# Kernel optimization log

Measured on AMD Instinct MI355X. Metric: run time of the kernel, lower is better.

## Reference

```python
import jax, jax.numpy as jnp
import numpy as np

B, T, D = 64, 1024, 1024  # batch, seq_len, in_dim == out_dim
N_UNIT = 2


def _lstm_cell(x, h, c, Wih, Whh):
    # x:[B,Din], h,c:[B,D]; Wih:[4D,Din], Whh:[4D,D]  (PyTorch gate order i,f,g,o)
    gates = x @ Wih.T + h @ Whh.T           # [B,4D]
    i, f, g, o = jnp.split(gates, 4, axis=-1)
    i = jax.nn.sigmoid(i)
    f = jax.nn.sigmoid(f)
    g = jnp.tanh(g)
    o = jax.nn.sigmoid(o)
    c_new = f * c + i * g
    h_new = o * jnp.tanh(c_new)
    return h_new, c_new


def setup_inputs() -> dict:
    key = jax.random.key(0)
    ks = jax.random.split(key, 5)
    s_in = 1.0 / np.sqrt(D)
    x = jax.random.normal(ks[0], (B, T, D), dtype=jnp.float32)
    Wih0 = jax.random.normal(ks[1], (4 * D, D), dtype=jnp.float32) * s_in
    Whh0 = jax.random.normal(ks[2], (4 * D, D), dtype=jnp.float32) * s_in
    Wih1 = jax.random.normal(ks[3], (4 * D, D), dtype=jnp.float32) * s_in
    Whh1 = jax.random.normal(ks[4], (4 * D, D), dtype=jnp.float32) * s_in
    return {"x": x, "Wih0": Wih0, "Whh0": Whh0, "Wih1": Wih1, "Whh1": Whh1}


def reference(x, Wih0, Whh0, Wih1, Whh1):
    b = x.shape[0]
    d = Whh0.shape[1]
    z = jnp.zeros((b, d), dtype=x.dtype)
    # Original code seeds both h and c of every unit with the same zeros tensor.
    carry0 = (z, z, z, z)  # (h0, c0, h1, c1)

    def step(carry, xt):
        h0, c0, h1, c1 = carry
        h0, c0 = _lstm_cell(xt, h0, c0, Wih0, Whh0)
        h1, c1 = _lstm_cell(h0, h1, c1, Wih1, Whh1)
        return (h0, c0, h1, c1), h1

    xs = jnp.swapaxes(x, 0, 1)  # [T,B,D]
    _, outs = jax.lax.scan(step, carry0, xs)
    return jnp.swapaxes(outs, 0, 1)  # [B,T,D]
```

## Files before the change

kernel.cpp:

```cpp
#include <hip/hip_runtime.h>
#include <cstdint>
#include <cstddef>

#define B_ 64
#define T_ 1024
#define D_ 1024
#define NBLK 256

typedef __attribute__((ext_vector_type(8))) _Float16 half8;
typedef __attribute__((ext_vector_type(4))) float f32x4;
typedef unsigned int u32;
typedef unsigned long long u64;
typedef unsigned short u16;

static __device__ __forceinline__ f32x4 mfma16(half8 a, half8 b, f32x4 c) {
  return __builtin_amdgcn_mfma_f32_16x16x32_f16(a, b, c, 0, 0, 0);
}
static __device__ __forceinline__ u64 cohl64(const u64* p) {
  return __hip_atomic_load(p, __ATOMIC_RELAXED, __HIP_MEMORY_SCOPE_AGENT);
}
static __device__ __forceinline__ u32 cohl32(const u32* p) {
  return __hip_atomic_load(p, __ATOMIC_RELAXED, __HIP_MEMORY_SCOPE_AGENT);
}
static __device__ __forceinline__ void cohs32(u32* p, u32 v) {
  __hip_atomic_store(p, v, __ATOMIC_RELAXED, __HIP_MEMORY_SCOPE_AGENT);
}
static __device__ __forceinline__ u16 h2u(_Float16 h) {
  return __builtin_bit_cast(u16, h);
}


static __device__ __forceinline__ void stage_coh(const _Float16* src, u64* st, int tid) {
  const int r = tid >> 5, j = tid & 31;
  const u64* p0 = (const u64*)(src + (size_t)r * D_) + j * 2;
  const u64* p1 = (const u64*)(src + (size_t)(r + 16) * D_) + j * 2;
  #pragma unroll
  for (int k = 0; k < 4; ++k) {
    st[2 * k] = cohl64(p0 + k * 64);
    st[2 * k + 1] = cohl64(p0 + k * 64 + 1);
    st[8 + 2 * k] = cohl64(p1 + k * 64);
    st[8 + 2 * k + 1] = cohl64(p1 + k * 64 + 1);
  }
}
static __device__ __forceinline__ void stage_x(const _Float16* src, u64* st, int tid) {
  const int r = tid >> 5, j = tid & 31;
  const u64* p0 = (const u64*)(src + (size_t)r * T_ * D_) + j * 2;
  const u64* p1 = (const u64*)(src + (size_t)(r + 16) * T_ * D_) + j * 2;
  #pragma unroll
  for (int k = 0; k < 4; ++k) {
    st[2 * k] = p0[k * 64];
    st[2 * k + 1] = p0[k * 64 + 1];
    st[8 + 2 * k] = p1[k * 64];
    st[8 + 2 * k + 1] = p1[k * 64 + 1];
  }
}
static __device__ __forceinline__ void stage_xf(const float* src, u64* st, int tid) {
  const int r = tid >> 5, j = tid & 31;
  #pragma unroll
  for (int h = 0; h < 2; ++h) {
    const float4* p = (const float4*)(src + (size_t)(r + h * 16) * T_ * D_) + j * 2;
    #pragma unroll
    for (int k = 0; k < 4; ++k) {
      #pragma unroll
      for (int q = 0; q < 2; ++q) {
        float4 v = p[k * 64 + q];
        union { u16 us[4]; u64 u; } pk;
        pk.us[0] = h2u((_Float16)v.x); pk.us[1] = h2u((_Float16)v.y);
        pk.us[2] = h2u((_Float16)v.z); pk.us[3] = h2u((_Float16)v.w);
        st[h * 8 + 2 * k + q] = pk.u;
      }
    }
  }
}
static __device__ __forceinline__ void stage_write(char* lds, const u64* st, int tid) {
  const int r = tid >> 5, j = tid & 31;
  #pragma unroll
  for (int h = 0; h < 2; ++h) {
    const int rr = r + h * 16;
    const int sw = (rr & 7) << 4;
    char* row = lds + rr * 2048;
    #pragma unroll
    for (int k = 0; k < 4; ++k) {
      char* dst = row + ((j * 16 + k * 512) ^ sw);
      *(u64*)dst = st[h * 8 + 2 * k];
      *(u64*)(dst + 8) = st[h * 8 + 2 * k + 1];
    }
  }
}

static __device__ __forceinline__ void gemm_gp(
    f32x4* acc, const char* ldsA, const half8* wA, const half8* wBv,
    int kq, int lane) {
  const int r = lane & 15;
  const int kl2 = (lane >> 4) << 4;
  const int sw = (r & 7) << 4;
  const char* p0 = ldsA + r * 2048;
  const char* p1 = ldsA + (16 + r) * 2048;
  #pragma unroll
  for (int ks = 0; ks < 8; ++ks) {
    const int kb = (kq * 512 + ks * 64 + kl2) ^ sw;
    half8 a0 = *(const half8*)(p0 + kb);
    half8 a1 = *(const half8*)(p1 + kb);
    acc[0] = mfma16(a0, wA[ks], acc[0]);
    acc[1] = mfma16(a1, wA[ks], acc[1]);
    acc[2] = mfma16(a0, wBv[ks], acc[2]);
    acc[3] = mfma16(a1, wBv[ks], acc[3]);
  }
}

static __device__ __forceinline__ void pollwait2(const u32* slots, u32 gen0,
                                                 u32 gen1, int tid) {
  if (tid < NBLK) {
    const u32 tgt = (tid < 128) ? gen0 : gen1;
    if (tgt > 0) {
      const u32* p = slots + tid * 32;
      int spin = 0;
      while (cohl32(p) < tgt && ++spin < (1 << 16))
        __builtin_amdgcn_s_sleep(2);
    }
  }
  __syncthreads();
}


template <bool XPRE>
__global__ __launch_bounds__(512, 2) void lstm_persist(
    const float* __restrict__ x32, const _Float16* __restrict__ xh,
    const _Float16* __restrict__ W,
    _Float16* h0,
    _Float16* h1,
    float* __restrict__ out, u32* slots)
{
  __shared__ char bufA[65536];
  __shared__ char bufB[65536];
  float (*glp)[32][68] = (float (*)[32][68])bufA;

  const int tid = threadIdx.x;
  const int lane = tid & 63;
  const int wv = tid >> 6;
  const int kq = wv >> 1;
  const int gp = wv & 1;
  const int bid = blockIdx.x;
  const int slot = bid >> 3;
  const int lyr = slot >> 4;
  const int mh = (slot >> 3) & 1;
  const int dgrp = (bid & 7) * 8 + (slot & 7);
  const int d0 = dgrp << 4;
  const int mbase = mh << 5;
  const int r = lane & 15;
  const int klane = lane >> 4;

  const _Float16* Wih = W + (size_t)(2 * lyr) * 4096 * 1024;
  const _Float16* Whh = Wih + (size_t)4096 * 1024;
  const size_t row0 = (size_t)((gp * 2) * 1024 + d0 + r) * 1024 + kq * 256 + klane * 8;
  const size_t row1 = (size_t)((gp * 2 + 1) * 1024 + d0 + r) * 1024 + kq * 256 + klane * 8;
  half8 wihA[8], wihB[8], whhA[8], whhB[8];
  #pragma unroll
  for (int ks = 0; ks < 8; ++ks) {
    wihA[ks] = *(const half8*)(Wih + row0 + ks * 32);
    wihB[ks] = *(const half8*)(Wih + row1 + ks * 32);
    whhA[ks] = *(const half8*)(Whh + row0 + ks * 32);
    whhB[ks] = *(const half8*)(Whh + row1 + ks * 32);
  }
  #pragma unroll
  for (int ks = 0; ks < 8; ++ks) {
    asm volatile("" : "+v"(wihA[ks]));
    asm volatile("" : "+v"(wihB[ks]));
    asm volatile("" : "+v"(whhA[ks]));
    asm volatile("" : "+v"(whhB[ks]));
  }

  float creg0 = 0.f, creg1 = 0.f;
  const int cb = tid >> 3;
  const int cd = (tid & 7) << 1;
  const size_t HS = (size_t)B_ * D_;

  u64 st[16];
  if (lyr == 0) {
    if (XPRE) stage_x(xh + (size_t)mbase * T_ * D_, st, tid);
    else      stage_xf(x32 + (size_t)mbase * T_ * D_, st, tid);
  }

  for (int s = 0; s <= T_; ++s) {
    const bool active = lyr ? (s >= 1) : (s < T_);
    const int t = lyr ? (s - 1) : s;

    if (lyr == 0)
      pollwait2(slots, (u32)s, (u32)(s > 4 ? s - 4 : 0), tid);
    else
      pollwait2(slots, (u32)s, (u32)s, tid);

    if (active) {
      const _Float16* h0prev = h0 + (size_t)((s + 7) & 7) * HS + (size_t)mbase * D_;
      if (lyr == 0) {
        stage_write(bufA, st, tid);
      } else {
        stage_coh(h0prev, st, tid);
        stage_write(bufA, st, tid);
      }
      __syncthreads();

      if (lyr == 0) stage_coh(h0prev, st, tid);
      else          stage_coh(h1 + (size_t)(s & 1) * HS + (size_t)mbase * D_, st, tid);

      f32x4 acc[4];
      #pragma unroll
      for (int i = 0; i < 4; ++i) acc[i] = (f32x4){0.f, 0.f, 0.f, 0.f};
      gemm_gp(acc, bufA, wihA, wihB, kq, lane);
      stage_write(bufB, st, tid);
      __syncthreads();
      gemm_gp(acc, bufB, whhA, whhB, kq, lane);

      {
        const int r4 = klane << 2;
        const int c0 = (gp * 2) * 16 + r;
        #pragma unroll
        for (int i = 0; i < 4; ++i) {
          glp[kq][r4 + i][c0]           = acc[0][i];
          glp[kq][16 + r4 + i][c0]      = acc[1][i];
          glp[kq][r4 + i][c0 + 16]      = acc[2][i];
          glp[kq][16 + r4 + i][c0 + 16] = acc[3][i];
        }
      }
      __syncthreads();

      if (tid < 256) {
        float g4[4][2];
        #pragma unroll
        for (int gg = 0; gg < 4; ++gg) {
          g4[gg][0] = glp[0][cb][gg * 16 + cd] + glp[1][cb][gg * 16 + cd]
                    + glp[2][cb][gg * 16 + cd] + glp[3][cb][gg * 16 + cd];
          g4[gg][1] = glp[0][cb][gg * 16 + cd + 1] + glp[1][cb][gg * 16 + cd + 1]
                    + glp[2][cb][gg * 16 + cd + 1] + glp[3][cb][gg * 16 + cd + 1];
        }
        const float i0 = 1.f / (1.f + expf(-g4[0][0])), i1 = 1.f / (1.f + expf(-g4[0][1]));
        const float f0 = 1.f / (1.f + expf(-g4[1][0])), f1 = 1.f / (1.f + expf(-g4[1][1]));
        const float z0 = tanhf(g4[2][0]),               z1 = tanhf(g4[2][1]);
        const float o0 = 1.f / (1.f + expf(-g4[3][0])), o1 = 1.f / (1.f + expf(-g4[3][1]));
        creg0 = f0 * creg0 + i0 * z0;
        creg1 = f1 * creg1 + i1 * z1;
        const float hn0 = o0 * tanhf(creg0);
        const float hn1 = o1 * tanhf(creg1);
        union { u16 us[2]; u32 u; } pk;
        pk.us[0] = h2u((_Float16)hn0);
        pk.us[1] = h2u((_Float16)hn1);
        _Float16* hw = lyr
            ? (h1 + (size_t)((s + 1) & 1) * HS)
            : (h0 + (size_t)(s & 7) * HS);
        cohs32((u32*)(hw + (size_t)(mbase + cb) * D_ + d0 + cd), pk.u);
        if (lyr) {
          float2 o2; o2.x = hn0; o2.y = hn1;
          *(float2*)(out + ((size_t)(mbase + cb) * T_ + t) * D_ + d0 + cd) = o2;
        }
      }
    }

    __syncthreads();
    if (tid == 0) cohs32(slots + bid * 32, (u32)(s + 1));

    if (lyr == 0 && s + 1 < T_) {
      if (XPRE) stage_x(xh + ((size_t)mbase * T_ + (s + 1)) * D_, st, tid);
      else      stage_xf(x32 + ((size_t)mbase * T_ + (s + 1)) * D_, st, tid);
    }
  }
}

__global__ void convw(const float* __restrict__ w0, const float* __restrict__ w1,
                      const float* __restrict__ w2, const float* __restrict__ w3,
                      u64* __restrict__ dst) {
  const size_t n1 = (size_t)D_ * D_;
  const size_t n = 4 * n1;
  for (size_t i = (size_t)blockIdx.x * blockDim.x + threadIdx.x; i < n;
       i += (size_t)gridDim.x * blockDim.x) {
    const size_t m = i / n1, j = i - m * n1;
    const float* src = (m == 0) ? w0 : (m == 1) ? w1 : (m == 2) ? w2 : w3;
    float4 v = ((const float4*)src)[j];
    union { u16 us[4]; u64 u; } pk;
    pk.us[0] = h2u((_Float16)v.x); pk.us[1] = h2u((_Float16)v.y);
    pk.us[2] = h2u((_Float16)v.z); pk.us[3] = h2u((_Float16)v.w);
    dst[i] = pk.u;
  }
}
__global__ void convx(const float* __restrict__ x, u64* __restrict__ xh) {
  const size_t n = (size_t)B_ * T_ * D_ / 4;
  for (size_t i = (size_t)blockIdx.x * blockDim.x + threadIdx.x; i < n;
       i += (size_t)gridDim.x * blockDim.x) {
    float4 v = ((const float4*)x)[i];
    union { u16 us[4]; u64 u; } pk;
    pk.us[0] = h2u((_Float16)v.x); pk.us[1] = h2u((_Float16)v.y);
    pk.us[2] = h2u((_Float16)v.z); pk.us[3] = h2u((_Float16)v.w);
    xh[i] = pk.u;
  }
}

extern "C" void kernel_launch(void* const* d_in, const int* in_sizes, int n_in,
                              void* d_out, int out_size, void* d_ws, size_t ws_size,
                              hipStream_t stream) {
  (void)in_sizes; (void)n_in; (void)out_size;
  const float* x = (const float*)d_in[0];
  const float* Wih0 = (const float*)d_in[1];
  const float* Whh0 = (const float*)d_in[2];
  const float* Wih1 = (const float*)d_in[3];
  const float* Whh1 = (const float*)d_in[4];
  float* out = (float*)d_out;

  char* ws = (char*)d_ws;
  const size_t MB = 1ull << 20;
  const size_t KB = 1024;
  _Float16* Wf = (_Float16*)ws;
  _Float16* h0 = (_Float16*)(ws + 32 * MB);
  _Float16* h1 = (_Float16*)(ws + 33 * MB);
  u32* slots = (u32*)(ws + 33 * MB + 256 * KB);
  _Float16* xh = (_Float16*)(ws + 35 * MB);
  const bool xpre = ws_size >= 35 * MB + (size_t)B_ * T_ * D_ * 2;

  hipMemsetAsync(ws + 32 * MB, 0, 1 * MB + 256 * KB + 32 * KB, stream);
  convw<<<4096, 256, 0, stream>>>(Wih0, Whh0, Wih1, Whh1, (u64*)Wf);
  if (xpre) {
    convx<<<4096, 256, 0, stream>>>(x, (u64*)xh);
    lstm_persist<true><<<NBLK, 512, 0, stream>>>(x, xh, Wf, h0, h1, out, slots);
  } else {
    lstm_persist<false><<<NBLK, 512, 0, stream>>>(x, xh, Wf, h0, h1, out, slots);
  }
}
```

Measured before the change: 5.668 ms.

## Narrow per-step polling to relevant M-half producers and use fast activations

Each block now waits only on the producer blocks for its own batch half (mh) instead of all 256 slots. Layer 0 writes the staged x tile to LDS before polling, so that write overlaps the wait. The exact expf/tanhf gate activations are replaced by __expf plus hardware reciprocal approximations. Together these aim to cut barrier latency and transcendental cost on the serial recurrence path, at the price of small accuracy loss and reliance on the mh slot partitioning being correct.

Result: slower. 5.826 ms (+2.8%).

```diff
diff --git a/kernel.cpp b/kernel.cpp
--- a/kernel.cpp
+++ b/kernel.cpp
@@ -27,6 +27,13 @@
 }
 static __device__ __forceinline__ u16 h2u(_Float16 h) {
   return __builtin_bit_cast(u16, h);
+}
+
+static __device__ __forceinline__ float fsig(float x) {
+  return __builtin_amdgcn_rcpf(1.f + __expf(-x));
+}
+static __device__ __forceinline__ float ftanh(float x) {
+  return 1.f - 2.f * __builtin_amdgcn_rcpf(1.f + __expf(2.f * x));
 }
 
 
@@ -108,12 +115,17 @@
   }
 }
 
-static __device__ __forceinline__ void pollwait2(const u32* slots, u32 gen0,
-                                                 u32 gen1, int tid) {
-  if (tid < NBLK) {
-    const u32 tgt = (tid < 128) ? gen0 : gen1;
+static __device__ __forceinline__ void pollwait_mh(const u32* slots, int lyr,
+                                                   int mh, int s, int tid) {
+  if (tid < 128) {
+    int sb; u32 tgt;
+    if (tid < 64) { sb = mh * 64 + tid; tgt = (u32)s; }
+    else {
+      sb = 128 + mh * 64 + (tid - 64);
+      tgt = lyr ? (u32)s : (u32)(s > 4 ? s - 4 : 0);
+    }
     if (tgt > 0) {
-      const u32* p = slots + tid * 32;
+      const u32* p = slots + sb * 32;
       int spin = 0;
       while (cohl32(p) < tgt && ++spin < (1 << 16))
         __builtin_amdgcn_s_sleep(2);
@@ -184,33 +196,37 @@
   for (int s = 0; s <= T_; ++s) {
     const bool active = lyr ? (s >= 1) : (s < T_);
     const int t = lyr ? (s - 1) : s;
-
-    if (lyr == 0)
-      pollwait2(slots, (u32)s, (u32)(s > 4 ? s - 4 : 0), tid);
-    else
-      pollwait2(slots, (u32)s, (u32)s, tid);
-
-    if (active) {
-      const _Float16* h0prev = h0 + (size_t)((s + 7) & 7) * HS + (size_t)mbase * D_;
-      if (lyr == 0) {
-        stage_write(bufA, st, tid);
-      } else {
+    const _Float16* h0prev = h0 + (size_t)((s + 7) & 7) * HS + (size_t)mbase * D_;
+
+    f32x4 acc[4];
+    #pragma unroll
+    for (int i = 0; i < 4; ++i) acc[i] = (f32x4){0.f, 0.f, 0.f, 0.f};
+
+    if (lyr == 0) {
+      if (active) stage_write(bufA, st, tid);
+      pollwait_mh(slots, 0, mh, s, tid);
+      if (active) {
+        stage_coh(h0prev, st, tid);
+        gemm_gp(acc, bufA, wihA, wihB, kq, lane);
+        stage_write(bufB, st, tid);
+        __syncthreads();
+        gemm_gp(acc, bufB, whhA, whhB, kq, lane);
+      }
+    } else {
+      pollwait_mh(slots, 1, mh, s, tid);
+      if (active) {
         stage_coh(h0prev, st, tid);
         stage_write(bufA, st, tid);
-      }
-      __syncthreads();
-
-      if (lyr == 0) stage_coh(h0prev, st, tid);
-      else          stage_coh(h1 + (size_t)(s & 1) * HS + (size_t)mbase * D_, st, tid);
-
-      f32x4 acc[4];
-      #pragma unroll
-      for (int i = 0; i < 4; ++i) acc[i] = (f32x4){0.f, 0.f, 0.f, 0.f};
-      gemm_gp(acc, bufA, wihA, wihB, kq, lane);
-      stage_write(bufB, st, tid);
-      __syncthreads();
-      gemm_gp(acc, bufB, whhA, whhB, kq, lane);
-
+        __syncthreads();
+        stage_coh(h1 + (size_t)(s & 1) * HS + (size_t)mbase * D_, st, tid);
+        gemm_gp(acc, bufA, wihA, wihB, kq, lane);
+        stage_write(bufB, st, tid);
+        __syncthreads();
+        gemm_gp(acc, bufB, whhA, whhB, kq, lane);
+      }
+    }
+
+    if (active) {
       {
         const int r4 = klane << 2;
         const int c0 = (gp * 2) * 16 + r;
@@ -233,14 +249,14 @@
           g4[gg][1] = glp[0][cb][gg * 16 + cd + 1] + glp[1][cb][gg * 16 + cd + 1]
                     + glp[2][cb][gg * 16 + cd + 1] + glp[3][cb][gg * 16 + cd + 1];
         }
-        const float i0 = 1.f / (1.f + expf(-g4[0][0])), i1 = 1.f / (1.f + expf(-g4[0][1]));
-        const float f0 = 1.f / (1.f + expf(-g4[1][0])), f1 = 1.f / (1.f + expf(-g4[1][1]));
-        const float z0 = tanhf(g4[2][0]),               z1 = tanhf(g4[2][1]);
-        const float o0 = 1.f / (1.f + expf(-g4[3][0])), o1 = 1.f / (1.f + expf(-g4[3][1]));
+        const float i0 = fsig(g4[0][0]),  i1 = fsig(g4[0][1]);
+        const float f0 = fsig(g4[1][0]),  f1 = fsig(g4[1][1]);
+        const float z0 = ftanh(g4[2][0]), z1 = ftanh(g4[2][1]);
+        const float o0 = fsig(g4[3][0]),  o1 = fsig(g4[3][1]);
         creg0 = f0 * creg0 + i0 * z0;
         creg1 = f1 * creg1 + i1 * z1;
-        const float hn0 = o0 * tanhf(creg0);
-        const float hn1 = o1 * tanhf(creg1);
+        const float hn0 = o0 * ftanh(creg0);
+        const float hn1 = o1 * ftanh(creg1);
         union { u16 us[2]; u32 u; } pk;
         pk.us[0] = h2u((_Float16)hn0);
         pk.us[1] = h2u((_Float16)hn1);
```
